# Kernel optimization log

Measured on AMD Instinct MI355X. Metric: run time of the kernel, lower is better.

Reference implementation:

```python
import jax, jax.numpy as jnp
import numpy as np

N_NODES = 100000

def gcn_conv(x, W, b, src, dst, n):
    # PyG GCNConv with add_self_loops=True, symmetric normalization.
    # Transform first (reduces feature dim before irregular aggregation).
    h = x @ W  # [N, out]
    # degree with self loops: in-degree over dst plus 1 per node
    deg = jax.ops.segment_sum(jnp.ones_like(dst, dtype=h.dtype), dst, num_segments=n) + 1.0
    dinv = jax.lax.rsqrt(deg)  # deg >= 1 due to self loops
    norm = dinv[src] * dinv[dst]  # [E]
    # message = norm * h[src], aggregated at dst; self-loop term = dinv_i^2 * h_i
    agg = jax.ops.segment_sum(h[src] * norm[:, None], dst, num_segments=n)
    agg = agg + h * (dinv * dinv)[:, None]
    return agg + b

def setup_inputs() -> dict:
    key = jax.random.key(0)
    k1, k2, k3, k4, k5 = jax.random.split(key, 5)
    F_in, H, E_dim = 128, 64, 64
    node_features = jax.random.normal(k1, (N_NODES, F_in), dtype=jnp.float32)
    edge_index = jax.random.randint(k2, (2, 1600000), 0, N_NODES, dtype=jnp.int64)
    s = 1.0 / np.sqrt(F_in)
    W1 = jax.random.uniform(k3, (F_in, H), jnp.float32, -s, s)
    b1 = jnp.zeros((H,), jnp.float32)
    s2 = 1.0 / np.sqrt(H)
    W2 = jax.random.uniform(k4, (H, H), jnp.float32, -s2, s2)
    b2 = jnp.zeros((H,), jnp.float32)
    Wl = jax.random.uniform(k5, (H, E_dim), jnp.float32, -s2, s2)
    bl = jnp.zeros((E_dim,), jnp.float32)
    return {"node_features": node_features, "edge_index": edge_index,
            "W1": W1, "b1": b1, "W2": W2, "b2": b2, "Wl": Wl, "bl": bl}

def reference(node_features, edge_index, W1, b1, W2, b2, Wl, bl):
    src, dst = edge_index[0], edge_index[1]
    n = node_features.shape[0]
    x = node_features.astype(jnp.float32)
    x = jax.nn.relu(gcn_conv(x, W1, b1, src, dst, n))
    # dropout: train=False -> identity
    x = jax.nn.relu(gcn_conv(x, W2, b2, src, dst, n))
    x = x @ Wl + bl
    return jax.nn.sigmoid(x).T  # [embed_size, N]
```

## Files before the change

### kernel.cpp

```cpp
#include <hip/hip_runtime.h>
#include <hip/hip_bf16.h>


#define FEAT 64
#define FIN 128
#define PAD 64
#define SUBC 4
#define SUBCAP 1280
#define CAP (SUBC * SUBCAP)
#define EPB 8192
#define MAXNB 512

typedef __attribute__((ext_vector_type(8))) short  short8;
typedef __attribute__((ext_vector_type(4))) float  f32x4;
typedef __attribute__((ext_vector_type(2))) float  float2v;

__device__ __forceinline__ unsigned short f2bf(float f) {
    union { float f; unsigned u; } x; x.f = f;
    unsigned r = x.u + 0x7FFF + ((x.u >> 16) & 1);
    return (unsigned short)(r >> 16);
}
__device__ __forceinline__ float bflo(unsigned u) {
    union { unsigned v; float f; } x; x.v = u << 16; return x.f;
}
__device__ __forceinline__ float bfhi(unsigned u) {
    union { unsigned v; float f; } x; x.v = u & 0xFFFF0000u; return x.f;
}

__global__ void wtrans_kernel(const float* __restrict__ W1, const float* __restrict__ W2,
                              const float* __restrict__ Wl,
                              unsigned short* __restrict__ Wt1, unsigned short* __restrict__ Wt2,
                              unsigned short* __restrict__ Wlt, int* __restrict__ bcnt) {
    int t = blockIdx.x * 256 + threadIdx.x;
    if (t < FIN * 64) {
        int k = t >> 6, n = t & 63;
        Wt1[n * FIN + k] = f2bf(W1[t]);
    } else if (t < FIN * 64 + 64 * 64) {
        int u = t - FIN * 64;
        int k = u >> 6, n = u & 63;
        Wt2[n * 64 + k] = f2bf(W2[u]);
    } else if (t < FIN * 64 + 2 * 64 * 64) {
        int u = t - FIN * 64 - 64 * 64;
        int k = u >> 6, n = u & 63;
        Wlt[n * 64 + k] = f2bf(Wl[u]);
    } else if (t < FIN * 64 + 2 * 64 * 64 + MAXNB * SUBC * 16) {
        bcnt[t - FIN * 64 - 2 * 64 * 64] = 0;
    }
}

__global__ __launch_bounds__(256) void bin_kernel(const int* __restrict__ ei,
                                                  int* __restrict__ bcnt,
                                                  int* __restrict__ bbuf,
                                                  int E, int nb) {
    __shared__ int hist[MAXNB];
    __shared__ int base[MAXNB];
    for (int t = threadIdx.x; t < nb; t += 256) hist[t] = 0;
    __syncthreads();
    int e0 = blockIdx.x * EPB;
    int sub = blockIdx.x & (SUBC - 1);
    int sreg[32], dreg[32], preg[32];
#pragma unroll
    for (int k = 0; k < 32; ++k) {
        int idx = e0 + k * 256 + threadIdx.x;
        if (idx < E) {
            sreg[k] = ei[idx];
            dreg[k] = ei[E + idx];
            preg[k] = atomicAdd(&hist[dreg[k] >> 8], 1);
        } else {
            dreg[k] = -1;
        }
    }
    __syncthreads();
    for (int t = threadIdx.x; t < nb; t += 256) {
        int h = hist[t];
        base[t] = (h > 0) ? atomicAdd(&bcnt[(t * SUBC + sub) * 16], h) : 0;
    }
    __syncthreads();
#pragma unroll
    for (int k = 0; k < 32; ++k) {
        if (dreg[k] >= 0) {
            int b = dreg[k] >> 8;
            int p = base[b] + preg[k];
            if (p < SUBCAP)
                bbuf[(size_t)b * CAP + sub * SUBCAP + p] = sreg[k] | ((dreg[k] & 255) << 20);
        }
    }
}

__global__ __launch_bounds__(256) void ell_from_bins_kernel(const int* __restrict__ bbuf,
                                                            const int* __restrict__ bcnt,
                                                            int* __restrict__ col,
                                                            int* __restrict__ cnt,
                                                            float* __restrict__ dinv,
                                                            unsigned int* __restrict__ gz,
                                                            int N) {
    __shared__ int lcnt[256];
    int b = blockIdx.x;
    int d0 = b << 8;
    lcnt[threadIdx.x] = 0;
    if (b == 0 && threadIdx.x < 32)
        gz[(size_t)N * 32 + threadIdx.x] = 0u;
    __syncthreads();
#pragma unroll
    for (int sub = 0; sub < SUBC; ++sub) {
        int ne = bcnt[(b * SUBC + sub) * 16];
        if (ne > SUBCAP) ne = SUBCAP;
        const int* eb = bbuf + (size_t)b * CAP + sub * SUBCAP;
        for (int i = threadIdx.x; i < ne; i += 256) {
            int w = eb[i];
            int s = w & 0xFFFFF;
            int dl = w >> 20;
            int slot = atomicAdd(&lcnt[dl], 1);
            if (slot < PAD) col[(size_t)(d0 + dl) * PAD + slot] = s;
        }
    }
    __syncthreads();
    int d = d0 + threadIdx.x;
    if (d < N) {
        int c = lcnt[threadIdx.x];
        if (c > PAD) c = PAD;
        int c8 = (c + 7) & ~7;
        for (int k = c; k < c8; ++k) col[(size_t)d * PAD + k] = N;
        cnt[d] = c;
        dinv[d] = rsqrtf((float)c + 1.0f);
    }
}

__global__ __launch_bounds__(256) void gemm1_mfma_kernel(const float* __restrict__ x,
                                                         const unsigned short* __restrict__ Wt,
                                                         const float* __restrict__ dinv,
                                                         unsigned short* __restrict__ g, int N) {
    const int lane = threadIdx.x & 63;
    const int wave = threadIdx.x >> 6;
    const int m = lane & 15, quad = lane >> 4;
    const int r0 = blockIdx.x * 64 + wave * 16;
    const int arow = r0 + m;
    const bool aok = arow < N;
    f32x4 acc[4] = {f32x4{0,0,0,0}, f32x4{0,0,0,0}, f32x4{0,0,0,0}, f32x4{0,0,0,0}};
    union { short8 s; unsigned short u[8]; } a;
#pragma unroll
    for (int s = 0; s < FIN / 32; ++s) {
        if (aok) {
            const float* xp = x + (size_t)arow * FIN + s * 32 + quad * 8;
            float4 a0 = *(const float4*)xp;
            float4 a1 = *(const float4*)(xp + 4);
            a.u[0] = f2bf(a0.x); a.u[1] = f2bf(a0.y);
            a.u[2] = f2bf(a0.z); a.u[3] = f2bf(a0.w);
            a.u[4] = f2bf(a1.x); a.u[5] = f2bf(a1.y);
            a.u[6] = f2bf(a1.z); a.u[7] = f2bf(a1.w);
        } else {
#pragma unroll
            for (int k = 0; k < 8; ++k) a.u[k] = 0;
        }
#pragma unroll
        for (int t = 0; t < 4; ++t) {
            const unsigned short* bp = Wt + (size_t)(t * 16 + m) * FIN + s * 32 + quad * 8;
            short8 bf = *(const short8*)bp;
            acc[t] = __builtin_amdgcn_mfma_f32_16x16x32_bf16(a.s, bf, acc[t], 0, 0, 0);
        }
    }
    const int rbase = r0 + quad * 4;
#pragma unroll
    for (int i = 0; i < 4; ++i) {
        int r = rbase + i;
        if (r < N) {
            float di = dinv[r];
#pragma unroll
            for (int t = 0; t < 4; ++t)
                g[(size_t)r * 64 + t * 16 + m] = f2bf(di * acc[t][i]);
        }
    }
}

__global__ __launch_bounds__(256) void gemm2_mfma_kernel(const unsigned short* __restrict__ xb,
                                                         const unsigned short* __restrict__ Wt,
                                                         const float* __restrict__ dinv,
                                                         unsigned short* __restrict__ g, int N) {
    const int lane = threadIdx.x & 63;
    const int wave = threadIdx.x >> 6;
    const int m = lane & 15, quad = lane >> 4;
    const int r0 = blockIdx.x * 64 + wave * 16;
    const int arow = r0 + m;
    const bool aok = arow < N;
    f32x4 acc[4] = {f32x4{0,0,0,0}, f32x4{0,0,0,0}, f32x4{0,0,0,0}, f32x4{0,0,0,0}};
    const short8 zero8 = short8{0,0,0,0,0,0,0,0};
#pragma unroll
    for (int s = 0; s < 2; ++s) {
        short8 a = aok ? *(const short8*)(xb + (size_t)arow * 64 + s * 32 + quad * 8) : zero8;
#pragma unroll
        for (int t = 0; t < 4; ++t) {
            short8 bf = *(const short8*)(Wt + (size_t)(t * 16 + m) * 64 + s * 32 + quad * 8);
            acc[t] = __builtin_amdgcn_mfma_f32_16x16x32_bf16(a, bf, acc[t], 0, 0, 0);
        }
    }
    const int rbase = r0 + quad * 4;
#pragma unroll
    for (int i = 0; i < 4; ++i) {
        int r = rbase + i;
        if (r < N) {
            float di = dinv[r];
#pragma unroll
            for (int t = 0; t < 4; ++t)
                g[(size_t)r * 64 + t * 16 + m] = f2bf(di * acc[t][i]);
        }
    }
}

__global__ __launch_bounds__(256) void agg_relu_kernel(const unsigned short* __restrict__ g,
                                                       const int* __restrict__ cnt,
                                                       const int* __restrict__ col,
                                                       const float* __restrict__ dinv,
                                                       const float* __restrict__ b,
                                                       unsigned short* __restrict__ xout, int N) {
    const int lane = threadIdx.x & 63;
    const int wave = threadIdx.x >> 6;
    const int ng = lane >> 3, fc = lane & 7;
    const int node = blockIdx.x * 32 + wave * 8 + ng;
    const bool valid = node < N;
    int c8 = 0;
    if (valid) {
        int c = cnt[node];
        if (c > PAD) c = PAD;
        c8 = (c + 7) & ~7;
    }
    int cmax = c8;
#pragma unroll
    for (int mk = 8; mk <= 32; mk <<= 1) {
        int o = __shfl_xor(cmax, mk, 64);
        cmax = cmax > o ? cmax : o;
    }
    const int* cl = col + (size_t)node * PAD;
    float2v acc0 = {0.f, 0.f}, acc1 = {0.f, 0.f}, acc2 = {0.f, 0.f}, acc3 = {0.f, 0.f};
    {
        uint4 w = *(const uint4*)(g + (size_t)(valid ? node : N) * 64 + fc * 8);
        acc0 += (float2v){bflo(w.x), bfhi(w.x)};
        acc1 += (float2v){bflo(w.y), bfhi(w.y)};
        acc2 += (float2v){bflo(w.z), bfhi(w.z)};
        acc3 += (float2v){bflo(w.w), bfhi(w.w)};
    }
    const int4 sent = {N, N, N, N};
    for (int j = 0; j < cmax; j += 8) {
        bool ok = j < c8;
        int4 ca = ok ? *(const int4*)(cl + j)     : sent;
        int4 cb = ok ? *(const int4*)(cl + j + 4) : sent;
        uint4 w0 = *(const uint4*)(g + (size_t)ca.x * 64 + fc * 8);
        uint4 w1 = *(const uint4*)(g + (size_t)ca.y * 64 + fc * 8);
        uint4 w2 = *(const uint4*)(g + (size_t)ca.z * 64 + fc * 8);
        uint4 w3 = *(const uint4*)(g + (size_t)ca.w * 64 + fc * 8);
        uint4 w4 = *(const uint4*)(g + (size_t)cb.x * 64 + fc * 8);
        uint4 w5 = *(const uint4*)(g + (size_t)cb.y * 64 + fc * 8);
        uint4 w6 = *(const uint4*)(g + (size_t)cb.z * 64 + fc * 8);
        uint4 w7 = *(const uint4*)(g + (size_t)cb.w * 64 + fc * 8);
        acc0 += (float2v){bflo(w0.x), bfhi(w0.x)};
        acc1 += (float2v){bflo(w0.y), bfhi(w0.y)};
        acc2 += (float2v){bflo(w0.z), bfhi(w0.z)};
        acc3 += (float2v){bflo(w0.w), bfhi(w0.w)};
        acc0 += (float2v){bflo(w1.x), bfhi(w1.x)};
        acc1 += (float2v){bflo(w1.y), bfhi(w1.y)};
        acc2 += (float2v){bflo(w1.z), bfhi(w1.z)};
        acc3 += (float2v){bflo(w1.w), bfhi(w1.w)};
        acc0 += (float2v){bflo(w2.x), bfhi(w2.x)};
        acc1 += (float2v){bflo(w2.y), bfhi(w2.y)};
        acc2 += (float2v){bflo(w2.z), bfhi(w2.z)};
        acc3 += (float2v){bflo(w2.w), bfhi(w2.w)};
        acc0 += (float2v){bflo(w3.x), bfhi(w3.x)};
        acc1 += (float2v){bflo(w3.y), bfhi(w3.y)};
        acc2 += (float2v){bflo(w3.z), bfhi(w3.z)};
        acc3 += (float2v){bflo(w3.w), bfhi(w3.w)};
        acc0 += (float2v){bflo(w4.x), bfhi(w4.x)};
        acc1 += (float2v){bflo(w4.y), bfhi(w4.y)};
        acc2 += (float2v){bflo(w4.z), bfhi(w4.z)};
        acc3 += (float2v){bflo(w4.w), bfhi(w4.w)};
        acc0 += (float2v){bflo(w5.x), bfhi(w5.x)};
        acc1 += (float2v){bflo(w5.y), bfhi(w5.y)};
        acc2 += (float2v){bflo(w5.z), bfhi(w5.z)};
        acc3 += (float2v){bflo(w5.w), bfhi(w5.w)};
        acc0 += (float2v){bflo(w6.x), bfhi(w6.x)};
        acc1 += (float2v){bflo(w6.y), bfhi(w6.y)};
        acc2 += (float2v){bflo(w6.z), bfhi(w6.z)};
        acc3 += (float2v){bflo(w6.w), bfhi(w6.w)};
        acc0 += (float2v){bflo(w7.x), bfhi(w7.x)};
        acc1 += (float2v){bflo(w7.y), bfhi(w7.y)};
        acc2 += (float2v){bflo(w7.z), bfhi(w7.z)};
        acc3 += (float2v){bflo(w7.w), bfhi(w7.w)};
    }
    if (valid) {
        float di = dinv[node];
        float4 b0 = *(const float4*)&b[fc * 8];
        float4 b1 = *(const float4*)&b[fc * 8 + 4];
        union { uint4 v; unsigned short u[8]; } o;
        o.u[0] = f2bf(fmaxf(di * acc0.x + b0.x, 0.f));
        o.u[1] = f2bf(fmaxf(di * acc0.y + b0.y, 0.f));
        o.u[2] = f2bf(fmaxf(di * acc1.x + b0.z, 0.f));
        o.u[3] = f2bf(fmaxf(di * acc1.y + b0.w, 0.f));
        o.u[4] = f2bf(fmaxf(di * acc2.x + b1.x, 0.f));
        o.u[5] = f2bf(fmaxf(di * acc2.y + b1.y, 0.f));
        o.u[6] = f2bf(fmaxf(di * acc3.x + b1.z, 0.f));
        o.u[7] = f2bf(fmaxf(di * acc3.y + b1.w, 0.f));
        *(uint4*)&xout[(size_t)node * 64 + fc * 8] = o.v;
    }
}

__global__ __launch_bounds__(256) void final_mfma_kernel(const unsigned short* __restrict__ x2,
                                                         const unsigned short* __restrict__ Wlt,
                                                         const float* __restrict__ bl,
                                                         float* __restrict__ out, int N) {
    const int lane = threadIdx.x & 63;
    const int wave = threadIdx.x >> 6;
    const int m = lane & 15, quad = lane >> 4;
    const int r0 = blockIdx.x * 64 + wave * 16;
    const int arow = r0 + m;
    const bool aok = arow < N;
    f32x4 acc[4] = {f32x4{0,0,0,0}, f32x4{0,0,0,0}, f32x4{0,0,0,0}, f32x4{0,0,0,0}};
    const short8 zero8 = short8{0,0,0,0,0,0,0,0};
#pragma unroll
    for (int s = 0; s < 2; ++s) {
        short8 a = aok ? *(const short8*)(x2 + (size_t)arow * 64 + s * 32 + quad * 8) : zero8;
#pragma unroll
        for (int t = 0; t < 4; ++t) {
            short8 bf = *(const short8*)(Wlt + (size_t)(t * 16 + m) * 64 + s * 32 + quad * 8);
            acc[t] = __builtin_amdgcn_mfma_f32_16x16x32_bf16(a, bf, acc[t], 0, 0, 0);
        }
    }
    const int rbase = r0 + quad * 4;
    if (rbase + 3 < N && (N & 3) == 0) {
#pragma unroll
        for (int t = 0; t < 4; ++t) {
            int j = t * 16 + m;
            float bj = bl[j];
            float4 o;
            o.x = 1.f / (1.f + __expf(-(acc[t][0] + bj)));
            o.y = 1.f / (1.f + __expf(-(acc[t][1] + bj)));
            o.z = 1.f / (1.f + __expf(-(acc[t][2] + bj)));
            o.w = 1.f / (1.f + __expf(-(acc[t][3] + bj)));
            *(float4*)&out[(size_t)j * N + rbase] = o;
        }
    } else {
#pragma unroll
        for (int t = 0; t < 4; ++t) {
            int j = t * 16 + m;
            float bj = bl[j];
#pragma unroll
            for (int i = 0; i < 4; ++i) {
                int r = rbase + i;
                if (r < N)
                    out[(size_t)j * N + r] = 1.f / (1.f + __expf(-(acc[t][i] + bj)));
            }
        }
    }
}

extern "C" void kernel_launch(void* const* d_in, const int* in_sizes, int n_in,
                              void* d_out, int out_size, void* d_ws, size_t ws_size,
                              hipStream_t stream) {
    const float* x   = (const float*)d_in[0];
    const int*   ei  = (const int*)d_in[1];
    const float* W1  = (const float*)d_in[2];
    const float* b1  = (const float*)d_in[3];
    const float* W2  = (const float*)d_in[4];
    const float* b2  = (const float*)d_in[5];
    const float* Wl  = (const float*)d_in[6];
    const float* bl  = (const float*)d_in[7];
    float*       out = (float*)d_out;

    int N  = in_sizes[0] / FIN;
    int E  = in_sizes[1] / 2;
    int nb = (N + 255) >> 8;
    int ng = (N + 63) >> 6;

    int*            bcnt = (int*)d_ws;
    unsigned short* Wt1  = (unsigned short*)(bcnt + MAXNB * SUBC * 16);
    unsigned short* Wt2  = Wt1 + FIN * 64;
    unsigned short* Wlt  = Wt2 + 64 * 64;
    int*            cnt  = (int*)(Wlt + 64 * 64);
    float*          dinv = (float*)(cnt + N);
    int*            col  = (int*)(dinv + N);
    int*            bbuf = col + (size_t)N * PAD;
    unsigned short* bufG = (unsigned short*)bbuf;
    unsigned short* bufX = bufG + (size_t)(N + 1) * FEAT;

    int wtot = FIN * 64 + 2 * 64 * 64 + MAXNB * SUBC * 16;
    wtrans_kernel<<<(wtot + 255) / 256, 256, 0, stream>>>(W1, W2, Wl, Wt1, Wt2, Wlt, bcnt);

    bin_kernel<<<(E + EPB - 1) / EPB, 256, 0, stream>>>(ei, bcnt, bbuf, E, nb);
    ell_from_bins_kernel<<<nb, 256, 0, stream>>>(bbuf, bcnt, col, cnt, dinv,
                                                 (unsigned int*)bufG, N);

    gemm1_mfma_kernel<<<ng, 256, 0, stream>>>(x, Wt1, dinv, bufG, N);
    agg_relu_kernel<<<(N + 31) / 32, 256, 0, stream>>>(bufG, cnt, col, dinv, b1, bufX, N);

    gemm2_mfma_kernel<<<ng, 256, 0, stream>>>(bufX, Wt2, dinv, bufG, N);
    agg_relu_kernel<<<(N + 31) / 32, 256, 0, stream>>>(bufG, cnt, col, dinv, b2, bufX, N);

    final_mfma_kernel<<<ng, 256, 0, stream>>>(bufX, Wlt, bl, out, N);
}
```

Before: 248.6 us.

## Fuse edge binning with first GEMM by moving source dinv scaling into aggregation

The first GEMM no longer depends on node degrees, because the source-side dinv scaling now happens inside the aggregation gather (a per-neighbor dinv lookup) rather than being baked into the GEMM output. That independence lets the edge-binning blocks and the first GEMM blocks share one launch and run concurrently, removing a kernel launch and the serialization between them. To avoid aliasing, the bin buffer gets its own workspace region, and a sentinel dinv[N]=0 is added for padded neighbors. The cost is an extra scattered 4-byte dinv load and multiply per edge in both aggregation passes.

```diff
diff --git a/kernel.cpp b/kernel.cpp
--- a/kernel.cpp
+++ b/kernel.cpp
@@ -48,41 +48,87 @@
     }
 }
 
-__global__ __launch_bounds__(256) void bin_kernel(const int* __restrict__ ei,
-                                                  int* __restrict__ bcnt,
-                                                  int* __restrict__ bbuf,
-                                                  int E, int nb) {
+__global__ __launch_bounds__(256) void bin_gemm1_kernel(const int* __restrict__ ei,
+                                                        int* __restrict__ bcnt,
+                                                        int* __restrict__ bbuf,
+                                                        const float* __restrict__ x,
+                                                        const unsigned short* __restrict__ Wt,
+                                                        unsigned short* __restrict__ g,
+                                                        int E, int nb, int nbb, int N) {
     __shared__ int hist[MAXNB];
     __shared__ int base[MAXNB];
-    for (int t = threadIdx.x; t < nb; t += 256) hist[t] = 0;
-    __syncthreads();
-    int e0 = blockIdx.x * EPB;
-    int sub = blockIdx.x & (SUBC - 1);
-    int sreg[32], dreg[32], preg[32];
-#pragma unroll
-    for (int k = 0; k < 32; ++k) {
-        int idx = e0 + k * 256 + threadIdx.x;
-        if (idx < E) {
-            sreg[k] = ei[idx];
-            dreg[k] = ei[E + idx];
-            preg[k] = atomicAdd(&hist[dreg[k] >> 8], 1);
-        } else {
-            dreg[k] = -1;
-        }
-    }
-    __syncthreads();
-    for (int t = threadIdx.x; t < nb; t += 256) {
-        int h = hist[t];
-        base[t] = (h > 0) ? atomicAdd(&bcnt[(t * SUBC + sub) * 16], h) : 0;
-    }
-    __syncthreads();
-#pragma unroll
-    for (int k = 0; k < 32; ++k) {
-        if (dreg[k] >= 0) {
-            int b = dreg[k] >> 8;
-            int p = base[b] + preg[k];
-            if (p < SUBCAP)
-                bbuf[(size_t)b * CAP + sub * SUBCAP + p] = sreg[k] | ((dreg[k] & 255) << 20);
+    if (blockIdx.x < (unsigned)nbb) {
+        for (int t = threadIdx.x; t < nb; t += 256) hist[t] = 0;
+        __syncthreads();
+        int e0 = blockIdx.x * EPB;
+        int sub = blockIdx.x & (SUBC - 1);
+        int sreg[32], dreg[32], preg[32];
+#pragma unroll
+        for (int k = 0; k < 32; ++k) {
+            int idx = e0 + k * 256 + threadIdx.x;
+            if (idx < E) {
+                sreg[k] = ei[idx];
+                dreg[k] = ei[E + idx];
+                preg[k] = atomicAdd(&hist[dreg[k] >> 8], 1);
+            } else {
+                dreg[k] = -1;
+            }
+        }
+        __syncthreads();
+        for (int t = threadIdx.x; t < nb; t += 256) {
+            int h = hist[t];
+            base[t] = (h > 0) ? atomicAdd(&bcnt[(t * SUBC + sub) * 16], h) : 0;
+        }
+        __syncthreads();
+#pragma unroll
+        for (int k = 0; k < 32; ++k) {
+            if (dreg[k] >= 0) {
+                int b = dreg[k] >> 8;
+                int p = base[b] + preg[k];
+                if (p < SUBCAP)
+                    bbuf[(size_t)b * CAP + sub * SUBCAP + p] = sreg[k] | ((dreg[k] & 255) << 20);
+            }
+        }
+    } else {
+        const int bid = blockIdx.x - nbb;
+        const int lane = threadIdx.x & 63;
+        const int wave = threadIdx.x >> 6;
+        const int m = lane & 15, quad = lane >> 4;
+        const int r0 = bid * 64 + wave * 16;
+        const int arow = r0 + m;
+        const bool aok = arow < N;
+        f32x4 acc[4] = {f32x4{0,0,0,0}, f32x4{0,0,0,0}, f32x4{0,0,0,0}, f32x4{0,0,0,0}};
+        union { short8 s; unsigned short u[8]; } a;
+#pragma unroll
+        for (int s = 0; s < FIN / 32; ++s) {
+            if (aok) {
+                const float* xp = x + (size_t)arow * FIN + s * 32 + quad * 8;
+                float4 a0 = *(const float4*)xp;
+                float4 a1 = *(const float4*)(xp + 4);
+                a.u[0] = f2bf(a0.x); a.u[1] = f2bf(a0.y);
+                a.u[2] = f2bf(a0.z); a.u[3] = f2bf(a0.w);
+                a.u[4] = f2bf(a1.x); a.u[5] = f2bf(a1.y);
+                a.u[6] = f2bf(a1.z); a.u[7] = f2bf(a1.w);
+            } else {
+#pragma unroll
+                for (int k = 0; k < 8; ++k) a.u[k] = 0;
+            }
+#pragma unroll
+            for (int t = 0; t < 4; ++t) {
+                const unsigned short* bp = Wt + (size_t)(t * 16 + m) * FIN + s * 32 + quad * 8;
+                short8 bf = *(const short8*)bp;
+                acc[t] = __builtin_amdgcn_mfma_f32_16x16x32_bf16(a.s, bf, acc[t], 0, 0, 0);
+            }
+        }
+        const int rbase = r0 + quad * 4;
+#pragma unroll
+        for (int i = 0; i < 4; ++i) {
+            int r = rbase + i;
+            if (r < N) {
+#pragma unroll
+                for (int t = 0; t < 4; ++t)
+                    g[(size_t)r * 64 + t * 16 + m] = f2bf(acc[t][i]);
+            }
         }
     }
 }
@@ -100,6 +146,7 @@
     lcnt[threadIdx.x] = 0;
     if (b == 0 && threadIdx.x < 32)
         gz[(size_t)N * 32 + threadIdx.x] = 0u;
+    if (b == 0 && threadIdx.x == 32) dinv[N] = 0.f;
     __syncthreads();
 #pragma unroll
     for (int sub = 0; sub < SUBC; ++sub) {
@@ -126,55 +173,8 @@
     }
 }
 
-__global__ __launch_bounds__(256) void gemm1_mfma_kernel(const float* __restrict__ x,
-                                                         const unsigned short* __restrict__ Wt,
-                                                         const float* __restrict__ dinv,
-                                                         unsigned short* __restrict__ g, int N) {
-    const int lane = threadIdx.x & 63;
-    const int wave = threadIdx.x >> 6;
-    const int m = lane & 15, quad = lane >> 4;
-    const int r0 = blockIdx.x * 64 + wave * 16;
-    const int arow = r0 + m;
-    const bool aok = arow < N;
-    f32x4 acc[4] = {f32x4{0,0,0,0}, f32x4{0,0,0,0}, f32x4{0,0,0,0}, f32x4{0,0,0,0}};
-    union { short8 s; unsigned short u[8]; } a;
-#pragma unroll
-    for (int s = 0; s < FIN / 32; ++s) {
-        if (aok) {
-            const float* xp = x + (size_t)arow * FIN + s * 32 + quad * 8;
-            float4 a0 = *(const float4*)xp;
-            float4 a1 = *(const float4*)(xp + 4);
-            a.u[0] = f2bf(a0.x); a.u[1] = f2bf(a0.y);
-            a.u[2] = f2bf(a0.z); a.u[3] = f2bf(a0.w);
-            a.u[4] = f2bf(a1.x); a.u[5] = f2bf(a1.y);
-            a.u[6] = f2bf(a1.z); a.u[7] = f2bf(a1.w);
-        } else {
-#pragma unroll
-            for (int k = 0; k < 8; ++k) a.u[k] = 0;
-        }
-#pragma unroll
-        for (int t = 0; t < 4; ++t) {
-            const unsigned short* bp = Wt + (size_t)(t * 16 + m) * FIN + s * 32 + quad * 8;
-            short8 bf = *(const short8*)bp;
-            acc[t] = __builtin_amdgcn_mfma_f32_16x16x32_bf16(a.s, bf, acc[t], 0, 0, 0);
-        }
-    }
-    const int rbase = r0 + quad * 4;
-#pragma unroll
-    for (int i = 0; i < 4; ++i) {
-        int r = rbase + i;
-        if (r < N) {
-            float di = dinv[r];
-#pragma unroll
-            for (int t = 0; t < 4; ++t)
-                g[(size_t)r * 64 + t * 16 + m] = f2bf(di * acc[t][i]);
-        }
-    }
-}
-
 __global__ __launch_bounds__(256) void gemm2_mfma_kernel(const unsigned short* __restrict__ xb,
                                                          const unsigned short* __restrict__ Wt,
-                                                         const float* __restrict__ dinv,
                                                          unsigned short* __restrict__ g, int N) {
     const int lane = threadIdx.x & 63;
     const int wave = threadIdx.x >> 6;
@@ -198,10 +198,9 @@
     for (int i = 0; i < 4; ++i) {
         int r = rbase + i;
         if (r < N) {
-            float di = dinv[r];
 #pragma unroll
             for (int t = 0; t < 4; ++t)
-                g[(size_t)r * 64 + t * 16 + m] = f2bf(di * acc[t][i]);
+                g[(size_t)r * 64 + t * 16 + m] = f2bf(acc[t][i]);
         }
     }
 }
@@ -217,6 +216,7 @@
     const int ng = lane >> 3, fc = lane & 7;
     const int node = blockIdx.x * 32 + wave * 8 + ng;
     const bool valid = node < N;
+    const float di = valid ? dinv[node] : 0.f;
     int c8 = 0;
     if (valid) {
         int c = cnt[node];
@@ -233,16 +233,18 @@
     float2v acc0 = {0.f, 0.f}, acc1 = {0.f, 0.f}, acc2 = {0.f, 0.f}, acc3 = {0.f, 0.f};
     {
         uint4 w = *(const uint4*)(g + (size_t)(valid ? node : N) * 64 + fc * 8);
-        acc0 += (float2v){bflo(w.x), bfhi(w.x)};
-        acc1 += (float2v){bflo(w.y), bfhi(w.y)};
-        acc2 += (float2v){bflo(w.z), bfhi(w.z)};
-        acc3 += (float2v){bflo(w.w), bfhi(w.w)};
+        acc0 += di * (float2v){bflo(w.x), bfhi(w.x)};
+        acc1 += di * (float2v){bflo(w.y), bfhi(w.y)};
+        acc2 += di * (float2v){bflo(w.z), bfhi(w.z)};
+        acc3 += di * (float2v){bflo(w.w), bfhi(w.w)};
     }
     const int4 sent = {N, N, N, N};
     for (int j = 0; j < cmax; j += 8) {
         bool ok = j < c8;
         int4 ca = ok ? *(const int4*)(cl + j)     : sent;
         int4 cb = ok ? *(const int4*)(cl + j + 4) : sent;
+        float e0 = dinv[ca.x], e1 = dinv[ca.y], e2 = dinv[ca.z], e3 = dinv[ca.w];
+        float e4 = dinv[cb.x], e5 = dinv[cb.y], e6 = dinv[cb.z], e7 = dinv[cb.w];
         uint4 w0 = *(const uint4*)(g + (size_t)ca.x * 64 + fc * 8);
         uint4 w1 = *(const uint4*)(g + (size_t)ca.y * 64 + fc * 8);
         uint4 w2 = *(const uint4*)(g + (size_t)ca.z * 64 + fc * 8);
@@ -251,41 +253,40 @@
         uint4 w5 = *(const uint4*)(g + (size_t)cb.y * 64 + fc * 8);
         uint4 w6 = *(const uint4*)(g + (size_t)cb.z * 64 + fc * 8);
         uint4 w7 = *(const uint4*)(g + (size_t)cb.w * 64 + fc * 8);
-        acc0 += (float2v){bflo(w0.x), bfhi(w0.x)};
-        acc1 += (float2v){bflo(w0.y), bfhi(w0.y)};
-        acc2 += (float2v){bflo(w0.z), bfhi(w0.z)};
-        acc3 += (float2v){bflo(w0.w), bfhi(w0.w)};
-        acc0 += (float2v){bflo(w1.x), bfhi(w1.x)};
-        acc1 += (float2v){bflo(w1.y), bfhi(w1.y)};
-        acc2 += (float2v){bflo(w1.z), bfhi(w1.z)};
-        acc3 += (float2v){bflo(w1.w), bfhi(w1.w)};
-        acc0 += (float2v){bflo(w2.x), bfhi(w2.x)};
-        acc1 += (float2v){bflo(w2.y), bfhi(w2.y)};
-        acc2 += (float2v){bflo(w2.z), bfhi(w2.z)};
-        acc3 += (float2v){bflo(w2.w), bfhi(w2.w)};
-        acc0 += (float2v){bflo(w3.x), bfhi(w3.x)};
-        acc1 += (float2v){bflo(w3.y), bfhi(w3.y)};
-        acc2 += (float2v){bflo(w3.z), bfhi(w3.z)};
-        acc3 += (float2v){bflo(w3.w), bfhi(w3.w)};
-        acc0 += (float2v){bflo(w4.x), bfhi(w4.x)};
-        acc1 += (float2v){bflo(w4.y), bfhi(w4.y)};
-        acc2 += (float2v){bflo(w4.z), bfhi(w4.z)};
-        acc3 += (float2v){bflo(w4.w), bfhi(w4.w)};
-        acc0 += (float2v){bflo(w5.x), bfhi(w5.x)};
-        acc1 += (float2v){bflo(w5.y), bfhi(w5.y)};
-        acc2 += (float2v){bflo(w5.z), bfhi(w5.z)};
-        acc3 += (float2v){bflo(w5.w), bfhi(w5.w)};
-        acc0 += (float2v){bflo(w6.x), bfhi(w6.x)};
-        acc1 += (float2v){bflo(w6.y), bfhi(w6.y)};
-        acc2 += (float2v){bflo(w6.z), bfhi(w6.z)};
-        acc3 += (float2v){bflo(w6.w), bfhi(w6.w)};
-        acc0 += (float2v){bflo(w7.x), bfhi(w7.x)};
-        acc1 += (float2v){bflo(w7.y), bfhi(w7.y)};
-        acc2 += (float2v){bflo(w7.z), bfhi(w7.z)};
-        acc3 += (float2v){bflo(w7.w), bfhi(w7.w)};
+        acc0 += e0 * (float2v){bflo(w0.x), bfhi(w0.x)};
+        acc1 += e0 * (float2v){bflo(w0.y), bfhi(w0.y)};
+        acc2 += e0 * (float2v){bflo(w0.z), bfhi(w0.z)};
+        acc3 += e0 * (float2v){bflo(w0.w), bfhi(w0.w)};
+        acc0 += e1 * (float2v){bflo(w1.x), bfhi(w1.x)};
+        acc1 += e1 * (float2v){bflo(w1.y), bfhi(w1.y)};
+        acc2 += e1 * (float2v){bflo(w1.z), bfhi(w1.z)};
+        acc3 += e1 * (float2v){bflo(w1.w), bfhi(w1.w)};
+        acc0 += e2 * (float2v){bflo(w2.x), bfhi(w2.x)};
+        acc1 += e2 * (float2v){bflo(w2.y), bfhi(w2.y)};
+        acc2 += e2 * (float2v){bflo(w2.z), bfhi(w2.z)};
+        acc3 += e2 * (float2v){bflo(w2.w), bfhi(w2.w)};
+        acc0 += e3 * (float2v){bflo(w3.x), bfhi(w3.x)};
+        acc1 += e3 * (float2v){bflo(w3.y), bfhi(w3.y)};
+        acc2 += e3 * (float2v){bflo(w3.z), bfhi(w3.z)};
+        acc3 += e3 * (float2v){bflo(w3.w), bfhi(w3.w)};
+        acc0 += e4 * (float2v){bflo(w4.x), bfhi(w4.x)};
+        acc1 += e4 * (float2v){bflo(w4.y), bfhi(w4.y)};
+        acc2 += e4 * (float2v){bflo(w4.z), bfhi(w4.z)};
+        acc3 += e4 * (float2v){bflo(w4.w), bfhi(w4.w)};
+        acc0 += e5 * (float2v){bflo(w5.x), bfhi(w5.x)};
+        acc1 += e5 * (float2v){bflo(w5.y), bfhi(w5.y)};
+        acc2 += e5 * (float2v){bflo(w5.z), bfhi(w5.z)};
+        acc3 += e5 * (float2v){bflo(w5.w), bfhi(w5.w)};
+        acc0 += e6 * (float2v){bflo(w6.x), bfhi(w6.x)};
+        acc1 += e6 * (float2v){bflo(w6.y), bfhi(w6.y)};
+        acc2 += e6 * (float2v){bflo(w6.z), bfhi(w6.z)};
+        acc3 += e6 * (float2v){bflo(w6.w), bfhi(w6.w)};
+        acc0 += e7 * (float2v){bflo(w7.x), bfhi(w7.x)};
+        acc1 += e7 * (float2v){bflo(w7.y), bfhi(w7.y)};
+        acc2 += e7 * (float2v){bflo(w7.z), bfhi(w7.z)};
+        acc3 += e7 * (float2v){bflo(w7.w), bfhi(w7.w)};
     }
     if (valid) {
-        float di = dinv[node];
         float4 b0 = *(const float4*)&b[fc * 8];
         float4 b1 = *(const float4*)&b[fc * 8 + 4];
         union { uint4 v; unsigned short u[8]; } o;
@@ -363,10 +364,11 @@
     const float* bl  = (const float*)d_in[7];
     float*       out = (float*)d_out;
 
-    int N  = in_sizes[0] / FIN;
-    int E  = in_sizes[1] / 2;
-    int nb = (N + 255) >> 8;
-    int ng = (N + 63) >> 6;
+    int N   = in_sizes[0] / FIN;
+    int E   = in_sizes[1] / 2;
+    int nb  = (N + 255) >> 8;
+    int nbb = (E + EPB - 1) / EPB;
+    int ng  = (N + 63) >> 6;
 
     int*            bcnt = (int*)d_ws;
     unsigned short* Wt1  = (unsigned short*)(bcnt + MAXNB * SUBC * 16);
@@ -374,22 +376,23 @@
     unsigned short* Wlt  = Wt2 + 64 * 64;
     int*            cnt  = (int*)(Wlt + 64 * 64);
     float*          dinv = (float*)(cnt + N);
-    int*            col  = (int*)(dinv + N);
-    int*            bbuf = col + (size_t)N * PAD;
-    unsigned short* bufG = (unsigned short*)bbuf;
+    int*            col  = (int*)(dinv + N + 4);
+    unsigned short* bufG = (unsigned short*)(col + (size_t)N * PAD);
     unsigned short* bufX = bufG + (size_t)(N + 1) * FEAT;
+    int*            bbuf = (int*)(bufX + (size_t)N * FEAT);
 
     int wtot = FIN * 64 + 2 * 64 * 64 + MAXNB * SUBC * 16;
     wtrans_kernel<<<(wtot + 255) / 256, 256, 0, stream>>>(W1, W2, Wl, Wt1, Wt2, Wlt, bcnt);
 
-    bin_kernel<<<(E + EPB - 1) / EPB, 256, 0, stream>>>(ei, bcnt, bbuf, E, nb);
+    bin_gemm1_kernel<<<nbb + ng, 256, 0, stream>>>(ei, bcnt, bbuf, x, Wt1, bufG,
+                                                   E, nb, nbb, N);
+
     ell_from_bins_kernel<<<nb, 256, 0, stream>>>(bbuf, bcnt, col, cnt, dinv,
                                                  (unsigned int*)bufG, N);
 
-    gemm1_mfma_kernel<<<ng, 256, 0, stream>>>(x, Wt1, dinv, bufG, N);
     agg_relu_kernel<<<(N + 31) / 32, 256, 0, stream>>>(bufG, cnt, col, dinv, b1, bufX, N);
 
-    gemm2_mfma_kernel<<<ng, 256, 0, stream>>>(bufX, Wt2, dinv, bufG, N);
+    gemm2_mfma_kernel<<<ng, 256, 0, stream>>>(bufX, Wt2, bufG, N);
     agg_relu_kernel<<<(N + 31) / 32, 256, 0, stream>>>(bufG, cnt, col, dinv, b2, bufX, N);
 
     final_mfma_kernel<<<ng, 256, 0, stream>>>(bufX, Wlt, bl, out, N);
```

New measurement: 286.0 us. 1.15x slower.

## Compute degrees up front and fuse edge binning with first GEMM launch

Applied to the files above, without the earlier changes.

Adds a separate degree-counting kernel that does global atomics per destination, so the first GEMM can compute the normalisation factor before the ELL build runs. Edge binning and the first MFMA GEMM now share one launch, with blocks split by index, so the two independent phases overlap on the GPU. The dinv array is removed and rsqrt is recomputed from cnt wherever it is needed. Bin packing keeps the slot and destination in one register and reloads src later, which lowers register pressure. In exchange it adds an extra full pass over dst with global atomics, and it moves bbuf so it no longer aliases bufG, which raises workspace use.

```diff
diff --git a/kernel.cpp b/kernel.cpp
--- a/kernel.cpp
+++ b/kernel.cpp
@@ -30,7 +30,8 @@
 __global__ void wtrans_kernel(const float* __restrict__ W1, const float* __restrict__ W2,
                               const float* __restrict__ Wl,
                               unsigned short* __restrict__ Wt1, unsigned short* __restrict__ Wt2,
-                              unsigned short* __restrict__ Wlt, int* __restrict__ bcnt) {
+                              unsigned short* __restrict__ Wlt, int* __restrict__ bcnt,
+                              int* __restrict__ cnt, int N) {
     int t = blockIdx.x * 256 + threadIdx.x;
     if (t < FIN * 64) {
         int k = t >> 6, n = t & 63;
@@ -45,44 +46,108 @@
         Wlt[n * 64 + k] = f2bf(Wl[u]);
     } else if (t < FIN * 64 + 2 * 64 * 64 + MAXNB * SUBC * 16) {
         bcnt[t - FIN * 64 - 2 * 64 * 64] = 0;
-    }
-}
-
-__global__ __launch_bounds__(256) void bin_kernel(const int* __restrict__ ei,
-                                                  int* __restrict__ bcnt,
-                                                  int* __restrict__ bbuf,
-                                                  int E, int nb) {
+    } else {
+        int u = t - FIN * 64 - 2 * 64 * 64 - MAXNB * SUBC * 16;
+        if (u < N) cnt[u] = 0;
+    }
+}
+
+__global__ __launch_bounds__(256) void deg_kernel(const int* __restrict__ ei,
+                                                  int* __restrict__ cnt, int E) {
+    int e0 = blockIdx.x * 2048;
+#pragma unroll
+    for (int k = 0; k < 8; ++k) {
+        int idx = e0 + k * 256 + threadIdx.x;
+        if (idx < E) atomicAdd(&cnt[ei[E + idx]], 1);
+    }
+}
+
+__global__ __launch_bounds__(256) void bin_gemm1_kernel(const int* __restrict__ ei,
+                                                        int* __restrict__ bcnt,
+                                                        int* __restrict__ bbuf,
+                                                        const float* __restrict__ x,
+                                                        const unsigned short* __restrict__ Wt,
+                                                        const int* __restrict__ cnt,
+                                                        unsigned short* __restrict__ g,
+                                                        int E, int nb, int nbb, int N) {
     __shared__ int hist[MAXNB];
     __shared__ int base[MAXNB];
-    for (int t = threadIdx.x; t < nb; t += 256) hist[t] = 0;
-    __syncthreads();
-    int e0 = blockIdx.x * EPB;
-    int sub = blockIdx.x & (SUBC - 1);
-    int sreg[32], dreg[32], preg[32];
-#pragma unroll
-    for (int k = 0; k < 32; ++k) {
-        int idx = e0 + k * 256 + threadIdx.x;
-        if (idx < E) {
-            sreg[k] = ei[idx];
-            dreg[k] = ei[E + idx];
-            preg[k] = atomicAdd(&hist[dreg[k] >> 8], 1);
-        } else {
-            dreg[k] = -1;
-        }
-    }
-    __syncthreads();
-    for (int t = threadIdx.x; t < nb; t += 256) {
-        int h = hist[t];
-        base[t] = (h > 0) ? atomicAdd(&bcnt[(t * SUBC + sub) * 16], h) : 0;
-    }
-    __syncthreads();
-#pragma unroll
-    for (int k = 0; k < 32; ++k) {
-        if (dreg[k] >= 0) {
-            int b = dreg[k] >> 8;
-            int p = base[b] + preg[k];
-            if (p < SUBCAP)
-                bbuf[(size_t)b * CAP + sub * SUBCAP + p] = sreg[k] | ((dreg[k] & 255) << 20);
+    if (blockIdx.x < (unsigned)nbb) {
+        for (int t = threadIdx.x; t < nb; t += 256) hist[t] = 0;
+        __syncthreads();
+        int e0 = blockIdx.x * EPB;
+        int sub = blockIdx.x & (SUBC - 1);
+        int pk[32];
+#pragma unroll
+        for (int k = 0; k < 32; ++k) {
+            int idx = e0 + k * 256 + threadIdx.x;
+            if (idx < E) {
+                int d = ei[E + idx];
+                int p = atomicAdd(&hist[d >> 8], 1);
+                pk[k] = (p << 17) | d;
+            } else {
+                pk[k] = -1;
+            }
+        }
+        __syncthreads();
+        for (int t = threadIdx.x; t < nb; t += 256) {
+            int h = hist[t];
+            base[t] = (h > 0) ? atomicAdd(&bcnt[(t * SUBC + sub) * 16], h) : 0;
+        }
+        __syncthreads();
+#pragma unroll
+        for (int k = 0; k < 32; ++k) {
+            if (pk[k] >= 0) {
+                int idx = e0 + k * 256 + threadIdx.x;
+                int s = ei[idx];
+                int d = pk[k] & 0x1FFFF;
+                int b = d >> 8;
+                int p = base[b] + ((unsigned)pk[k] >> 17);
+                if (p < SUBCAP)
+                    bbuf[(size_t)b * CAP + sub * SUBCAP + p] = s | ((d & 255) << 20);
+            }
+        }
+    } else {
+        const int bid = blockIdx.x - nbb;
+        const int lane = threadIdx.x & 63;
+        const int wave = threadIdx.x >> 6;
+        const int m = lane & 15, quad = lane >> 4;
+        const int r0 = bid * 64 + wave * 16;
+        const int arow = r0 + m;
+        const bool aok = arow < N;
+        f32x4 acc[4] = {f32x4{0,0,0,0}, f32x4{0,0,0,0}, f32x4{0,0,0,0}, f32x4{0,0,0,0}};
+        union { short8 s; unsigned short u[8]; } a;
+#pragma unroll
+        for (int s = 0; s < FIN / 32; ++s) {
+            if (aok) {
+                const float* xp = x + (size_t)arow * FIN + s * 32 + quad * 8;
+                float4 a0 = *(const float4*)xp;
+                float4 a1 = *(const float4*)(xp + 4);
+                a.u[0] = f2bf(a0.x); a.u[1] = f2bf(a0.y);
+                a.u[2] = f2bf(a0.z); a.u[3] = f2bf(a0.w);
+                a.u[4] = f2bf(a1.x); a.u[5] = f2bf(a1.y);
+                a.u[6] = f2bf(a1.z); a.u[7] = f2bf(a1.w);
+            } else {
+#pragma unroll
+                for (int k = 0; k < 8; ++k) a.u[k] = 0;
+            }
+#pragma unroll
+            for (int t = 0; t < 4; ++t) {
+                const unsigned short* bp = Wt + (size_t)(t * 16 + m) * FIN + s * 32 + quad * 8;
+                short8 bf = *(const short8*)bp;
+                acc[t] = __builtin_amdgcn_mfma_f32_16x16x32_bf16(a.s, bf, acc[t], 0, 0, 0);
+            }
+        }
+        const int rbase = r0 + quad * 4;
+#pragma unroll
+        for (int i = 0; i < 4; ++i) {
+            int r = rbase + i;
+            if (r < N) {
+                float di = rsqrtf((float)cnt[r] + 1.0f);
+#pragma unroll
+                for (int t = 0; t < 4; ++t)
+                    g[(size_t)r * 64 + t * 16 + m] = f2bf(di * acc[t][i]);
+            }
         }
     }
 }
@@ -91,7 +156,6 @@
                                                             const int* __restrict__ bcnt,
                                                             int* __restrict__ col,
                                                             int* __restrict__ cnt,
-                                                            float* __restrict__ dinv,
                                                             unsigned int* __restrict__ gz,
                                                             int N) {
     __shared__ int lcnt[256];
@@ -118,63 +182,16 @@
     int d = d0 + threadIdx.x;
     if (d < N) {
         int c = lcnt[threadIdx.x];
+        cnt[d] = c;
         if (c > PAD) c = PAD;
         int c8 = (c + 7) & ~7;
         for (int k = c; k < c8; ++k) col[(size_t)d * PAD + k] = N;
-        cnt[d] = c;
-        dinv[d] = rsqrtf((float)c + 1.0f);
-    }
-}
-
-__global__ __launch_bounds__(256) void gemm1_mfma_kernel(const float* __restrict__ x,
-                                                         const unsigned short* __restrict__ Wt,
-                                                         const float* __restrict__ dinv,
-                                                         unsigned short* __restrict__ g, int N) {
-    const int lane = threadIdx.x & 63;
-    const int wave = threadIdx.x >> 6;
-    const int m = lane & 15, quad = lane >> 4;
-    const int r0 = blockIdx.x * 64 + wave * 16;
-    const int arow = r0 + m;
-    const bool aok = arow < N;
-    f32x4 acc[4] = {f32x4{0,0,0,0}, f32x4{0,0,0,0}, f32x4{0,0,0,0}, f32x4{0,0,0,0}};
-    union { short8 s; unsigned short u[8]; } a;
-#pragma unroll
-    for (int s = 0; s < FIN / 32; ++s) {
-        if (aok) {
-            const float* xp = x + (size_t)arow * FIN + s * 32 + quad * 8;
-            float4 a0 = *(const float4*)xp;
-            float4 a1 = *(const float4*)(xp + 4);
-            a.u[0] = f2bf(a0.x); a.u[1] = f2bf(a0.y);
-            a.u[2] = f2bf(a0.z); a.u[3] = f2bf(a0.w);
-            a.u[4] = f2bf(a1.x); a.u[5] = f2bf(a1.y);
-            a.u[6] = f2bf(a1.z); a.u[7] = f2bf(a1.w);
-        } else {
-#pragma unroll
-            for (int k = 0; k < 8; ++k) a.u[k] = 0;
-        }
-#pragma unroll
-        for (int t = 0; t < 4; ++t) {
-            const unsigned short* bp = Wt + (size_t)(t * 16 + m) * FIN + s * 32 + quad * 8;
-            short8 bf = *(const short8*)bp;
-            acc[t] = __builtin_amdgcn_mfma_f32_16x16x32_bf16(a.s, bf, acc[t], 0, 0, 0);
-        }
-    }
-    const int rbase = r0 + quad * 4;
-#pragma unroll
-    for (int i = 0; i < 4; ++i) {
-        int r = rbase + i;
-        if (r < N) {
-            float di = dinv[r];
-#pragma unroll
-            for (int t = 0; t < 4; ++t)
-                g[(size_t)r * 64 + t * 16 + m] = f2bf(di * acc[t][i]);
-        }
     }
 }
 
 __global__ __launch_bounds__(256) void gemm2_mfma_kernel(const unsigned short* __restrict__ xb,
                                                          const unsigned short* __restrict__ Wt,
-                                                         const float* __restrict__ dinv,
+                                                         const int* __restrict__ cnt,
                                                          unsigned short* __restrict__ g, int N) {
     const int lane = threadIdx.x & 63;
     const int wave = threadIdx.x >> 6;
@@ -198,7 +215,7 @@
     for (int i = 0; i < 4; ++i) {
         int r = rbase + i;
         if (r < N) {
-            float di = dinv[r];
+            float di = rsqrtf((float)cnt[r] + 1.0f);
 #pragma unroll
             for (int t = 0; t < 4; ++t)
                 g[(size_t)r * 64 + t * 16 + m] = f2bf(di * acc[t][i]);
@@ -209,7 +226,6 @@
 __global__ __launch_bounds__(256) void agg_relu_kernel(const unsigned short* __restrict__ g,
                                                        const int* __restrict__ cnt,
                                                        const int* __restrict__ col,
-                                                       const float* __restrict__ dinv,
                                                        const float* __restrict__ b,
                                                        unsigned short* __restrict__ xout, int N) {
     const int lane = threadIdx.x & 63;
@@ -218,8 +234,10 @@
     const int node = blockIdx.x * 32 + wave * 8 + ng;
     const bool valid = node < N;
     int c8 = 0;
+    float di = 0.f;
     if (valid) {
         int c = cnt[node];
+        di = rsqrtf((float)c + 1.0f);
         if (c > PAD) c = PAD;
         c8 = (c + 7) & ~7;
     }
@@ -285,7 +303,6 @@
         acc3 += (float2v){bflo(w7.w), bfhi(w7.w)};
     }
     if (valid) {
-        float di = dinv[node];
         float4 b0 = *(const float4*)&b[fc * 8];
         float4 b1 = *(const float4*)&b[fc * 8 + 4];
         union { uint4 v; unsigned short u[8]; } o;
@@ -363,34 +380,38 @@
     const float* bl  = (const float*)d_in[7];
     float*       out = (float*)d_out;
 
-    int N  = in_sizes[0] / FIN;
-    int E  = in_sizes[1] / 2;
-    int nb = (N + 255) >> 8;
-    int ng = (N + 63) >> 6;
+    int N   = in_sizes[0] / FIN;
+    int E   = in_sizes[1] / 2;
+    int nb  = (N + 255) >> 8;
+    int nbb = (E + EPB - 1) / EPB;
+    int ng  = (N + 63) >> 6;
 
     int*            bcnt = (int*)d_ws;
     unsigned short* Wt1  = (unsigned short*)(bcnt + MAXNB * SUBC * 16);
     unsigned short* Wt2  = Wt1 + FIN * 64;
     unsigned short* Wlt  = Wt2 + 64 * 64;
     int*            cnt  = (int*)(Wlt + 64 * 64);
-    float*          dinv = (float*)(cnt + N);
-    int*            col  = (int*)(dinv + N);
-    int*            bbuf = col + (size_t)N * PAD;
-    unsigned short* bufG = (unsigned short*)bbuf;
+    int*            col  = cnt + N;
+    unsigned short* bufG = (unsigned short*)(col + (size_t)N * PAD);
     unsigned short* bufX = bufG + (size_t)(N + 1) * FEAT;
-
-    int wtot = FIN * 64 + 2 * 64 * 64 + MAXNB * SUBC * 16;
-    wtrans_kernel<<<(wtot + 255) / 256, 256, 0, stream>>>(W1, W2, Wl, Wt1, Wt2, Wlt, bcnt);
-
-    bin_kernel<<<(E + EPB - 1) / EPB, 256, 0, stream>>>(ei, bcnt, bbuf, E, nb);
-    ell_from_bins_kernel<<<nb, 256, 0, stream>>>(bbuf, bcnt, col, cnt, dinv,
+    int*            bbuf = (int*)(bufX + (size_t)N * FEAT);
+
+    int wtot = FIN * 64 + 2 * 64 * 64 + MAXNB * SUBC * 16 + N;
+    wtrans_kernel<<<(wtot + 255) / 256, 256, 0, stream>>>(W1, W2, Wl, Wt1, Wt2, Wlt,
+                                                          bcnt, cnt, N);
+
+    deg_kernel<<<(E + 2047) / 2048, 256, 0, stream>>>(ei, cnt, E);
+
+    bin_gemm1_kernel<<<nbb + ng, 256, 0, stream>>>(ei, bcnt, bbuf, x, Wt1, cnt, bufG,
+                                                   E, nb, nbb, N);
+
+    ell_from_bins_kernel<<<nb, 256, 0, stream>>>(bbuf, bcnt, col, cnt,
                                                  (unsigned int*)bufG, N);
 
-    gemm1_mfma_kernel<<<ng, 256, 0, stream>>>(x, Wt1, dinv, bufG, N);
-    agg_relu_kernel<<<(N + 31) / 32, 256, 0, stream>>>(bufG, cnt, col, dinv, b1, bufX, N);
-
-    gemm2_mfma_kernel<<<ng, 256, 0, stream>>>(bufX, Wt2, dinv, bufG, N);
-    agg_relu_kernel<<<(N + 31) / 32, 256, 0, stream>>>(bufG, cnt, col, dinv, b2, bufX, N);
+    agg_relu_kernel<<<(N + 31) / 32, 256, 0, stream>>>(bufG, cnt, col, b1, bufX, N);
+
+    gemm2_mfma_kernel<<<ng, 256, 0, stream>>>(bufX, Wt2, cnt, bufG, N);
+    agg_relu_kernel<<<(N + 31) / 32, 256, 0, stream>>>(bufG, cnt, col, b2, bufX, N);
 
     final_mfma_kernel<<<ng, 256, 0, stream>>>(bufX, Wlt, bl, out, N);
 }
```

Measured after the change: 317.6 us. +27.8%, slower.
